# Optimization experiments

Hardware: AMD Instinct MI355X
Metric: run time of the kernel (lower is better)

The kernel has to match this reference:

```python
import jax, jax.numpy as jnp
import numpy as np
from jax import lax

EPS = 1e-05
Q = 4          # window size (hard-coded in BotBlock)
HEADS = 4
DIM = 16       # bottleneck(64) // heads(4)


def conv3x3(x, w, b):
    # x: [N,C,H,W], w: [O,I,3,3]
    y = lax.conv_general_dilated(x, w, (1, 1), ((1, 1), (1, 1)),
                                 dimension_numbers=('NCHW', 'OIHW', 'NCHW'))
    return y + b[None, :, None, None]


def batchnorm(x, gamma, beta):
    # training-mode BN: batch statistics over (N,H,W), biased variance
    m = jnp.mean(x, axis=(0, 2, 3), keepdims=True)
    v = jnp.var(x, axis=(0, 2, 3), keepdims=True)
    xn = (x - m) * lax.rsqrt(v + EPS)
    return xn * gamma[None, :, None, None] + beta[None, :, None, None]


def rel_to_abs(x):
    # x: [B, H, L, 2L-1] -> [B, H, L, L] via pad/reshape trick
    B, H, L, _ = x.shape
    x = jnp.pad(x, ((0, 0), (0, 0), (0, 0), (0, 1)))          # [B,H,L,2L]
    flat = x.reshape(B, H, -1)                                  # [B,H,2L*L]
    flat = jnp.pad(flat, ((0, 0), (0, 0), (0, L - 1)))
    final = flat.reshape(B, H, L + 1, 2 * L - 1)
    return final[:, :, :L, L - 1:]                              # [B,H,L,L]


def relative_logits_1d(q, rel_k, perm):
    # q: [b, n, h, w, d], rel_k: [2w-1, d]
    b, n, h, w, d = q.shape
    rl = jnp.einsum('bnhwd,md->bnhwm', q, rel_k)
    rl = rl.reshape(b, n * h, w, 2 * w - 1)
    rl = rel_to_abs(rl)                                         # [b, n*h, w, w]
    rl = rl.reshape(b, n, h, w, w)
    rl = jnp.broadcast_to(rl[:, :, :, None], (b, n, h, h, w, w))
    return jnp.transpose(rl, perm)


def rel_pos_attention(q, k, v, rel_w, rel_h):
    # q,k,v: [b, heads, h, w, d]
    b, n, h, w, d = q.shape
    q = q * (d ** -0.5)
    logits = jnp.einsum('bnhwd,bnpqd->bnhwpq', q, k)
    logits = logits + relative_logits_1d(q, rel_w, (0, 1, 2, 4, 3, 5))
    logits = logits + relative_logits_1d(jnp.transpose(q, (0, 1, 3, 2, 4)),
                                         rel_h, (0, 1, 4, 2, 5, 3))
    weights = jax.nn.softmax(logits.reshape(b, n, h, w, h * w), axis=-1)
    weights = weights.reshape(b, n, h, w, h, w)
    out = jnp.einsum('bnhwpq,bnpqd->bhwnd', weights, v)         # [b,h,w,n,d]
    return out.reshape(b, h, w, n * d)                          # fold heads


def setup_inputs() -> dict:
    key = jax.random.key(0)
    ks = jax.random.split(key, 16)
    C_in, C_bot, C_out = 64, 64, 256
    inp = {
        'x': jax.random.normal(ks[0], (2, C_in, 256, 256), jnp.float32),
        'conv1_w': jax.random.normal(ks[1], (C_bot, C_in, 3, 3), jnp.float32) * 0.05,
        'conv1_b': jnp.zeros((C_bot,), jnp.float32),
        'bn1_g': jnp.ones((C_bot,), jnp.float32),
        'bn1_b': jnp.zeros((C_bot,), jnp.float32),
        'wq': jax.random.normal(ks[2], (C_bot, HEADS, DIM), jnp.float32) * 0.01,
        'wk': jax.random.normal(ks[3], (C_bot, HEADS, DIM), jnp.float32) * 0.01,
        'wv': jax.random.normal(ks[4], (C_bot, HEADS, DIM), jnp.float32) * 0.01,
        'rel_w': jax.random.normal(ks[5], (2 * Q - 1, DIM), jnp.float32) * (DIM ** -0.5),
        'rel_h': jax.random.normal(ks[6], (2 * Q - 1, DIM), jnp.float32) * (DIM ** -0.5),
        'bn2_g': jnp.ones((C_bot,), jnp.float32),
        'bn2_b': jnp.zeros((C_bot,), jnp.float32),
        'conv3_w': jax.random.normal(ks[7], (C_out, C_bot, 3, 3), jnp.float32) * 0.05,
        'conv3_b': jnp.zeros((C_out,), jnp.float32),
        # NOTE: original init_zero=True zeros bn3 gamma; we randomize it so the
        # output (and gradients) are non-trivial for kernel correctness checks.
        'bn3_g': jax.random.normal(ks[8], (C_out,), jnp.float32),
        'bn3_b': jnp.zeros((C_out,), jnp.float32),
    }
    return inp


def reference(x, conv1_w, conv1_b, bn1_g, bn1_b, wq, wk, wv, rel_w, rel_h,
              bn2_g, bn2_b, conv3_w, conv3_b, bn3_g, bn3_b):
    N, C, H, W = x.shape
    P_h, P_w = H // Q, W // Q
    # raw memory reinterpretation into 4x4 blocks (matches torch .reshape)
    xb = x.reshape(N * P_h * P_w, C, Q, Q)
    out = jax.nn.relu(batchnorm(conv3x3(xb, conv1_w, conv1_b), bn1_g, bn1_b))
    # GroupPointWise projections: NCHW -> NHWC then einsum
    feat = jnp.transpose(out, (0, 2, 3, 1))                     # [b,h,w,c]
    q = jnp.einsum('bhwc,cnp->bnhwp', feat, wq)
    k = jnp.einsum('bhwc,cnp->bnhwp', feat, wk)
    v = jnp.einsum('bhwc,cnp->bnhwp', feat, wv)
    o = rel_pos_attention(q, k, v, rel_w, rel_h)                # [b,h,w,c]
    o = jnp.transpose(o, (0, 3, 1, 2))                          # NCHW
    o = jax.nn.relu(batchnorm(o, bn2_g, bn2_b))
    o = batchnorm(conv3x3(o, conv3_w, conv3_b), bn3_g, bn3_b)   # no act
    C1 = o.shape[1]
    o = o.reshape(N, C1, H, W)
    return jax.nn.relu(o)
```

## Files before the change

kernel.cpp:

```cpp
#include <hip/hip_runtime.h>
#include <stdint.h>


#define EPSV 1e-5f
#define INV_N (1.0f / 131072.0f)

typedef unsigned short u16;
typedef __attribute__((ext_vector_type(8))) short short8b;
typedef __attribute__((ext_vector_type(4))) short short4b;
typedef __attribute__((ext_vector_type(4))) float f32x4;

__device__ __forceinline__ u16 f2bf(float f) {
  unsigned u = __float_as_uint(f);
  u += 0x7fffu + ((u >> 16) & 1u);
  return (u16)(u >> 16);
}
__device__ __forceinline__ float bf2f(u16 h) {
  return __uint_as_float((unsigned)h << 16);
}
__device__ __forceinline__ unsigned cvtpk(float lo, float hi) {
  unsigned r;
  asm("v_cvt_pk_bf16_f32 %0, %1, %2" : "=v"(r) : "v"(lo), "v"(hi));
  return r;
}
__device__ __forceinline__ short4b pack4(unsigned lo, unsigned hi) {
  union { unsigned u[2]; short4b s; } x;
  x.u[0] = lo; x.u[1] = hi;
  return x.s;
}
__device__ __forceinline__ f32x4 mfma16(short4b a, short4b b, f32x4 c) {
#if __has_builtin(__builtin_amdgcn_mfma_f32_16x16x16_bf16)
  return __builtin_amdgcn_mfma_f32_16x16x16_bf16(a, b, c, 0, 0, 0);
#elif __has_builtin(__builtin_amdgcn_mfma_f32_16x16x16bf16_1k)
  return __builtin_amdgcn_mfma_f32_16x16x16bf16_1k(a, b, c, 0, 0, 0);
#else
  f32x4 d;
  asm volatile("v_mfma_f32_16x16x16_bf16 %0, %1, %2, %3\n\ts_nop 7\n\ts_nop 7"
               : "=v"(d) : "v"(a), "v"(b), "v"(c));
  return d;
#endif
}

__device__ __forceinline__ float bn_scale(const float* __restrict__ acc,
                                          const float* __restrict__ gam,
                                          const float* __restrict__ bet,
                                          int C, int c, float& shift) {
  float S = acc[c], S2 = acc[C + c];
  float mean = S * INV_N;
  float var  = S2 * INV_N - mean * mean;
  float rstd = rsqrtf(var + EPSV);
  float sc = gam[c] * rstd;
  shift = bet[c] - mean * sc;
  return sc;
}

__global__ __launch_bounds__(256) void prep_kernel(const float* __restrict__ w1,
                                                   const float* __restrict__ w3,
                                                   const float* __restrict__ wq,
                                                   const float* __restrict__ wk,
                                                   const float* __restrict__ wv,
                                                   const float* __restrict__ relw,
                                                   const float* __restrict__ relh,
                                                   u16* __restrict__ wp1,
                                                   u16* __restrict__ wp3,
                                                   u16* __restrict__ wqkvT) {
  int i = blockIdx.x * 256 + threadIdx.x;
  const int tot1 = 18 * 64 * 40;
  const int tot3 = 9 * 256 * 64;
  if (i < tot1) {
    int ch = i / (64 * 40); int r = i - ch * 64 * 40; int o = r / 40; int kk = r - o * 40;
    float v = 0.f;
    if (kk < 32) { int k = ch * 32 + kk; int tap = k >> 6; int c = k & 63;
                   v = w1[o * 576 + c * 9 + tap]; }
    wp1[i] = f2bf(v);
  } else if (i < tot1 + tot3) {
    int j = i - tot1;
    int tap = j >> 14; int r = j & 16383; int o = r >> 6; int c = r & 63;
    wp3[j] = f2bf(w3[o * 576 + c * 9 + tap]);
  } else if (i < tot1 + tot3 + 192 * 64) {
    int j = i - tot1 - tot3;
    int oc = j >> 6, c = j & 63;
    const float* src = (oc < 64) ? wq : (oc < 128) ? wk : wv;
    float v = src[(c << 6) + (oc & 63)];
    if (oc < 64) v *= 0.25f;
    wqkvT[j] = f2bf(v);
  } else if (i < tot1 + tot3 + 192 * 64 + 4096) {
    int j = i - tot1 - tot3 - 192 * 64;
    int c = j & 63; int col = (j >> 6) & 31; int tbl = j >> 11;
    int n = col >> 3, m = col & 7;
    float v = 0.f;
    if (m < 7) {
      const float* rel = tbl ? relh : relw;
#pragma unroll
      for (int d = 0; d < 16; ++d) v += wq[c * 64 + n * 16 + d] * rel[m * 16 + d];
      v *= 0.25f;
    }
    wqkvT[(192 + tbl * 32 + col) * 64 + c] = f2bf(v);
  }
}

__global__ __launch_bounds__(256) void conv1_kernel(const float* __restrict__ x,
                                                    const u16* __restrict__ wp,
                                                    u16* __restrict__ bufb,
                                                    float* __restrict__ partials1) {
  __shared__ __align__(16) char featA[257 * 128];
  __shared__ __align__(16) char ldsW[2][64 * 80];
  const int t = threadIdx.x;
  const int lane = t & 63, w = t >> 6;
  const int lrow = lane & 15, lk = lane >> 4;
  const int wm = w >> 1, wn = w & 1;
  const size_t Mbase = (size_t)blockIdx.x * 256;

  int rel[9];
  {
    const int pi = lrow >> 2, pj = lrow & 3;
#pragma unroll
    for (int tap = 0; tap < 9; ++tap) {
      const int ti = tap / 3, tj = tap - ti * 3;
      int si = pi + ti - 1, sj = pj + tj - 1;
      bool valid = ((unsigned)si < 4u) && ((unsigned)sj < 4u);
      rel[tap] = valid ? ((si * 4 + sj) << 7) : (1 << 24);
    }
  }

  {
    const int cp = t >> 3, ph = t & 7;
    const int gsw = ((cp >> 2) << 4) | ((cp & 3) << 2);
#pragma unroll
    for (int i = 0; i < 16; ++i) {
      const float* bp = x + Mbase * 64 + i * 1024 + cp * 32 + ph * 2;
      float2 a = *reinterpret_cast<const float2*>(bp);
      float2 b = *reinterpret_cast<const float2*>(bp + 16);
#pragma unroll
      for (int j = 0; j < 2; ++j) {
        const int row = i * 16 + ph * 2 + j;
        unsigned pk = cvtpk(j ? a.y : a.x, j ? b.y : b.x);
        const int byte = row * 128 + (gsw ^ ((row & 7) << 4));
        *reinterpret_cast<unsigned*>(featA + byte) = pk;
      }
    }
  }
  if (t < 8) *reinterpret_cast<uint4*>(featA + 256 * 128 + t * 16) = uint4{0, 0, 0, 0};

  uint4 s0, s1;
  {
    const u16* sp = wp;
    s0 = *reinterpret_cast<const uint4*>(sp + (size_t)t * 8);
    if (t < 64) s1 = *reinterpret_cast<const uint4*>(sp + (size_t)(t + 256) * 8);
    *reinterpret_cast<uint4*>(ldsW[0] + t * 16) = s0;
    if (t < 64) *reinterpret_cast<uint4*>(ldsW[0] + (t + 256) * 16) = s1;
  }
  __syncthreads();

  f32x4 acc[8][2] = {};
#pragma unroll
  for (int chn = 0; chn < 18; ++chn) {
    const int cur = chn & 1;
    const int tap = chn >> 1, kk = chn & 1;
    if (chn + 1 < 18) {
      const u16* sp = wp + (chn + 1) * 2560;
      s0 = *reinterpret_cast<const uint4*>(sp + (size_t)t * 8);
      if (t < 64) s1 = *reinterpret_cast<const uint4*>(sp + (size_t)(t + 256) * 8);
    }
    const int kkg = (kk << 6) | (lk << 4);
    short8b bw[2];
#pragma unroll
    for (int n = 0; n < 2; ++n)
      bw[n] = *reinterpret_cast<const short8b*>(ldsW[cur] + (wn * 32 + n * 16 + lrow) * 80 + lk * 16);
#pragma unroll
    for (int m = 0; m < 8; ++m) {
      int ad = ((wm * 128 + m * 16) << 7) + rel[tap];
      ad = ad < 32768 ? ad : 32768;
      ad += (kkg ^ ((ad >> 3) & 0x70));
      short8b af = *reinterpret_cast<const short8b*>(featA + ad);
#pragma unroll
      for (int n = 0; n < 2; ++n)
        acc[m][n] = __builtin_amdgcn_mfma_f32_16x16x32_bf16(af, bw[n], acc[m][n], 0, 0, 0);
    }
    if (chn + 1 < 18) {
      *reinterpret_cast<uint4*>(ldsW[cur ^ 1] + t * 16) = s0;
      if (t < 64) *reinterpret_cast<uint4*>(ldsW[cur ^ 1] + (t + 256) * 16) = s1;
    }
    __syncthreads();
  }

#pragma unroll
  for (int m = 0; m < 8; ++m) {
    const size_t rowg0 = Mbase + wm * 128 + m * 16 + lk * 4;
#pragma unroll
    for (int n = 0; n < 2; ++n) {
      const int o = wn * 32 + n * 16 + lrow;
#pragma unroll
      for (int r = 0; r < 4; ++r)
        bufb[(rowg0 + r) * 64 + o] = f2bf(acc[m][n][r]);
    }
  }

  float* pst = reinterpret_cast<float*>(featA);
  if (t < 128) pst[t] = 0.f;
  __syncthreads();
#pragma unroll
  for (int n = 0; n < 2; ++n) {
    float s = 0.f, s2 = 0.f;
#pragma unroll
    for (int m = 0; m < 8; ++m)
#pragma unroll
      for (int r = 0; r < 4; ++r) {
        float v = acc[m][n][r];
        s += v; s2 = fmaf(v, v, s2);
      }
    s += __shfl_xor(s, 16); s2 += __shfl_xor(s2, 16);
    s += __shfl_xor(s, 32); s2 += __shfl_xor(s2, 32);
    if (lk == 0) {
      const int o = wn * 32 + n * 16 + lrow;
      atomicAdd(&pst[o], s);
      atomicAdd(&pst[64 + o], s2);
    }
  }
  __syncthreads();
  if (t < 128) partials1[(size_t)blockIdx.x * 128 + t] = pst[t];
}

__global__ __launch_bounds__(256) void reduce12_kernel(const float* __restrict__ p,
                                                       float* __restrict__ acc, int nrows) {
  const int c = blockIdx.x, t = threadIdx.x;
  float s = 0.f;
  for (int i = t; i < nrows; i += 256) s += p[(size_t)i * 128 + c];
#pragma unroll
  for (int off = 32; off > 0; off >>= 1) s += __shfl_down(s, off);
  __shared__ float red[4];
  if ((t & 63) == 0) red[t >> 6] = s;
  __syncthreads();
  if (t == 0) acc[c] = red[0] + red[1] + red[2] + red[3];
}

__global__ __launch_bounds__(256) void attn_kernel(u16* __restrict__ buf,
                                                   const u16* __restrict__ wqkvT,
                                                   const float* __restrict__ acc1,
                                                   const float* __restrict__ g1,
                                                   const float* __restrict__ b1,
                                                   float* __restrict__ partials2) {
  __shared__ float scsh[64][2];
  __shared__ float pstA[128];
  __shared__ __align__(16) u16 feat_l[4][1024];
  __shared__ __align__(16) float S_lds[4][16 * 18];
  __shared__ __align__(16) u16 V_lds[4][16 * 20];
  __shared__ __align__(16) float inv_lds[4][16];
  __shared__ __align__(16) u16 rLs[4][1152];
  const int t = threadIdx.x, u = t >> 6, lane = t & 63;
  const size_t b = (size_t)blockIdx.x * 4 + u;
  const int lrow = lane & 15, lk = lane >> 4;
  float* Sl = S_lds[u];
  u16* Vl = V_lds[u];
  float* invl = inv_lds[u];
  u16* rL = rLs[u];

  if (t < 64) {
    float sh; float sc = bn_scale(acc1, g1, b1, 64, t, sh);
    scsh[t][0] = sc; scsh[t][1] = sh;
  }
  if (t < 128) pstA[t] = 0.f;
  __syncthreads();

  {
    const int pos = lane >> 2, cq = lane & 3;
    const u16* src = buf + b * 1024 + pos * 64 + cq * 16;
    short8b v0 = *reinterpret_cast<const short8b*>(src);
    short8b v1 = *reinterpret_cast<const short8b*>(src + 8);
    float f[16];
#pragma unroll
    for (int j = 0; j < 8; ++j) {
      const int c0 = cq * 16 + j, c1 = cq * 16 + 8 + j;
      f[j]     = fmaxf(fmaf(bf2f((u16)v0[j]), scsh[c0][0], scsh[c0][1]), 0.f);
      f[8 + j] = fmaxf(fmaf(bf2f((u16)v1[j]), scsh[c1][0], scsh[c1][1]), 0.f);
    }
    uint4 q0{cvtpk(f[0], f[1]), cvtpk(f[2], f[3]), cvtpk(f[4], f[5]), cvtpk(f[6], f[7])};
    uint4 q1{cvtpk(f[8], f[9]), cvtpk(f[10], f[11]), cvtpk(f[12], f[13]), cvtpk(f[14], f[15])};
    const int g0 = (cq * 2) ^ (pos & 7), g1g = (cq * 2 + 1) ^ (pos & 7);
    *reinterpret_cast<uint4*>(&feat_l[u][pos * 64 + g0 * 8]) = q0;
    *reinterpret_cast<uint4*>(&feat_l[u][pos * 64 + g1g * 8]) = q1;
  }

  short8b bfeat[2];
#pragma unroll
  for (int ch = 0; ch < 2; ++ch) {
    const int kg = ch * 4 + lk;
    bfeat[ch] = *reinterpret_cast<const short8b*>(&feat_l[u][lrow * 64 + ((kg ^ (lrow & 7)) * 8)]);
  }
  short4b qf[4], kf[4];
  uint2 vf[4];
#pragma unroll
  for (int ct = 0; ct < 16; ++ct) {
    f32x4 d = {0.f, 0.f, 0.f, 0.f};
#pragma unroll
    for (int ch = 0; ch < 2; ++ch) {
      short8b wfr = *reinterpret_cast<const short8b*>(&wqkvT[(ct * 16 + lrow) * 64 + ch * 32 + lk * 8]);
      d = __builtin_amdgcn_mfma_f32_16x16x32_bf16(wfr, bfeat[ch], d, 0, 0, 0);
    }
    if (ct < 4) {
      qf[ct] = pack4(cvtpk(d[0], d[1]), cvtpk(d[2], d[3]));
    } else if (ct < 8) {
      kf[ct - 4] = pack4(cvtpk(d[0], d[1]), cvtpk(d[2], d[3]));
    } else if (ct < 12) {
      vf[ct - 8] = uint2{cvtpk(d[0], d[1]), cvtpk(d[2], d[3])};
    } else {
#pragma unroll
      for (int r = 0; r < 4; ++r) {
        const int rc = (ct - 12) * 16 + lk * 4 + r;
        const int tbl = rc >> 5, col = rc & 31;
        rL[tbl * 576 + (col >> 3) * 144 + lrow * 9 + (col & 7)] = f2bf(d[r]);
      }
    }
  }

  const f32x4 fzero = {0.f, 0.f, 0.f, 0.f};
  const int qj3 = 3 - (lrow & 3);
  const int qi = lrow >> 2;
#pragma unroll
  for (int n = 0; n < 4; ++n) {
    f32x4 S = mfma16(qf[n], kf[n], fzero);
#pragma unroll
    for (int r = 0; r < 4; ++r) Sl[(lk * 4 + r) * 18 + lrow] = S[r];
    const float* srow = Sl + lrow * 18 + lk * 4;
    float2 sa = *reinterpret_cast<const float2*>(srow);
    float2 sb = *reinterpret_cast<const float2*>(srow + 2);
    float s0 = sa.x, s1 = sa.y, s2 = sb.x, s3 = sb.y;
    const u16* rwp = rL + n * 144 + lrow * 9 + qj3;
    const float rh = bf2f(rL[576 + n * 144 + lrow * 9 + 3 + lk - qi]);
    s0 += bf2f(rwp[0]) + rh; s1 += bf2f(rwp[1]) + rh;
    s2 += bf2f(rwp[2]) + rh; s3 += bf2f(rwp[3]) + rh;
    float m = fmaxf(fmaxf(s0, s1), fmaxf(s2, s3));
    m = fmaxf(m, __shfl_xor(m, 16)); m = fmaxf(m, __shfl_xor(m, 32));
    float p0 = __expf(s0 - m), p1 = __expf(s1 - m);
    float p2 = __expf(s2 - m), p3 = __expf(s3 - m);
    float ls = p0 + p1 + p2 + p3;
    ls += __shfl_xor(ls, 16); ls += __shfl_xor(ls, 32);
    if (lk == 0) invl[lrow] = 1.f / ls;
    short4b pf = pack4(cvtpk(p0, p1), cvtpk(p2, p3));
    *reinterpret_cast<uint2*>(Vl + lrow * 20 + lk * 4) = vf[n];
    const int vb = lk * 4;
    unsigned v0 = Vl[(vb + 0) * 20 + lrow], v1 = Vl[(vb + 1) * 20 + lrow];
    unsigned v2 = Vl[(vb + 2) * 20 + lrow], v3 = Vl[(vb + 3) * 20 + lrow];
    short4b vB = pack4(v0 | (v1 << 16), v2 | (v3 << 16));
    f32x4 O = mfma16(pf, vB, fzero);
    float4 iv = *reinterpret_cast<const float4*>(invl + lk * 4);
    float o0 = O[0] * iv.x, o1 = O[1] * iv.y, o2 = O[2] * iv.z, o3 = O[3] * iv.w;
    u16* ob = buf + b * 1024 + (n << 4) + lrow;
    ob[(lk * 4 + 0) * 64] = f2bf(o0); ob[(lk * 4 + 1) * 64] = f2bf(o1);
    ob[(lk * 4 + 2) * 64] = f2bf(o2); ob[(lk * 4 + 3) * 64] = f2bf(o3);
    float ss = o0 + o1 + o2 + o3;
    float s2s = o0 * o0 + o1 * o1 + o2 * o2 + o3 * o3;
    ss += __shfl_xor(ss, 16); s2s += __shfl_xor(s2s, 16);
    ss += __shfl_xor(ss, 32); s2s += __shfl_xor(s2s, 32);
    if (lk == 0) {
      atomicAdd(&pstA[(n << 4) + lrow], ss);
      atomicAdd(&pstA[64 + (n << 4) + lrow], s2s);
    }
  }
  __syncthreads();
  if (t < 128) partials2[(size_t)blockIdx.x * 128 + t] = pstA[t];
}

__global__ __launch_bounds__(256, 2) void conv3_kernel(const u16* __restrict__ src,
                                                       const u16* __restrict__ wp,
                                                       const float* __restrict__ acc2,
                                                       const float* __restrict__ g2,
                                                       const float* __restrict__ b2,
                                                       u16* __restrict__ y3b,
                                                       float* __restrict__ partials3) {
  __shared__ __align__(16) u16 featB[257 * 64];
  __shared__ __align__(16) u16 ldsW[2][128 * 64];
  __shared__ float scsh[128];
  __shared__ __align__(16) u16 Tl[4][16 * 20];
  const int t = threadIdx.x;
  const int lane = t & 63, w = t >> 6;
  const int lrow = lane & 15, lk = lane >> 4;
  const int wm = w >> 1, wn = w & 1;
  const int Nbase = blockIdx.x * 256;
  const int ohalf = blockIdx.y;

  int rel[9];
  {
    const int pi = lrow >> 2, pj = lrow & 3;
#pragma unroll
    for (int tap = 0; tap < 9; ++tap) {
      const int ti = tap / 3, tj = tap - ti * 3;
      int si = pi + ti - 1, sj = pj + tj - 1;
      bool valid = ((unsigned)si < 4u) && ((unsigned)sj < 4u);
      rel[tap] = valid ? ((si * 4 + sj) << 7) : (1 << 24);
    }
  }
  if (t < 64) {
    float sh; float sc = bn_scale(acc2, g2, b2, 64, t, sh);
    scsh[t * 2] = sc; scsh[t * 2 + 1] = sh;
  }
  const int so = t >> 1, shalf = t & 1, so7 = so & 7;
  {
    const u16* wsrc = wp + ohalf * 8192 + so * 64 + shalf * 32;
    uint4 w0 = *reinterpret_cast<const uint4*>(wsrc);
    uint4 w1 = *reinterpret_cast<const uint4*>(wsrc + 8);
    uint4 w2 = *reinterpret_cast<const uint4*>(wsrc + 16);
    uint4 w3v = *reinterpret_cast<const uint4*>(wsrc + 24);
    char* dst = (char*)ldsW[0] + so * 128;
    const int gb = shalf * 4;
    *reinterpret_cast<uint4*>(dst + (((gb + 0) ^ so7) << 4)) = w0;
    *reinterpret_cast<uint4*>(dst + (((gb + 1) ^ so7) << 4)) = w1;
    *reinterpret_cast<uint4*>(dst + (((gb + 2) ^ so7) << 4)) = w2;
    *reinterpret_cast<uint4*>(dst + (((gb + 3) ^ so7) << 4)) = w3v;
  }
  __syncthreads();
  {
    const u16* srow = src + (size_t)(Nbase + t) * 64;
    char* drow = (char*)featB + t * 128;
    const int r7 = t & 7;
#pragma unroll
    for (int g = 0; g < 8; ++g) {
      short8b v = *reinterpret_cast<const short8b*>(srow + g * 8);
      float f[8];
#pragma unroll
      for (int j = 0; j < 8; ++j) {
        const int c = g * 8 + j;
        f[j] = fmaxf(fmaf(bf2f((u16)v[j]), scsh[c * 2], scsh[c * 2 + 1]), 0.f);
      }
      uint4 pk{cvtpk(f[0], f[1]), cvtpk(f[2], f[3]), cvtpk(f[4], f[5]), cvtpk(f[6], f[7])};
      *reinterpret_cast<uint4*>(drow + ((g ^ r7) << 4)) = pk;
    }
  }
  if (t < 8) *reinterpret_cast<uint4*>((char*)featB + 32768 + t * 16) = uint4{0, 0, 0, 0};
  uint4 r0, r1, r2, r3v;
  {
    const u16* wsrc = wp + 16384 + ohalf * 8192 + so * 64 + shalf * 32;
    r0 = *reinterpret_cast<const uint4*>(wsrc);
    r1 = *reinterpret_cast<const uint4*>(wsrc + 8);
    r2 = *reinterpret_cast<const uint4*>(wsrc + 16);
    r3v = *reinterpret_cast<const uint4*>(wsrc + 24);
  }
  __syncthreads();
  f32x4 acc[4][8] = {};
  const char* fB = (const char*)featB;
  const int swzA0 = (lk << 4) ^ ((lrow & 7) << 4);
  const int swzA1 = (64 | (lk << 4)) ^ ((lrow & 7) << 4);
#pragma unroll
  for (int tap = 0; tap < 9; ++tap) {
    const int cur = tap & 1;
    const char* lW = (const char*)ldsW[cur];
    short8b aw0[4], aw1[4];
#pragma unroll
    for (int m = 0; m < 4; ++m) {
      const int rowoff = (wm * 64 + m * 16 + lrow) << 7;
      aw0[m] = *reinterpret_cast<const short8b*>(lW + rowoff + swzA0);
      aw1[m] = *reinterpret_cast<const short8b*>(lW + rowoff + swzA1);
    }
#pragma unroll
    for (int n = 0; n < 8; ++n) {
      int ad0 = ((wn * 128 + n * 16) << 7) + rel[tap];
      ad0 = ad0 < 32768 ? ad0 : 32768;
      const int swz = (ad0 >> 3) & 0x70;
      short8b bf0 = *reinterpret_cast<const short8b*>(fB + ad0 + ((lk << 4) ^ swz));
      short8b bf1 = *reinterpret_cast<const short8b*>(fB + ad0 + ((64 | (lk << 4)) ^ swz));
#pragma unroll
      for (int m = 0; m < 4; ++m) {
        acc[m][n] = __builtin_amdgcn_mfma_f32_16x16x32_bf16(aw0[m], bf0, acc[m][n], 0, 0, 0);
        acc[m][n] = __builtin_amdgcn_mfma_f32_16x16x32_bf16(aw1[m], bf1, acc[m][n], 0, 0, 0);
      }
    }
    if (tap < 8) {
      char* dst = (char*)ldsW[cur ^ 1] + so * 128;
      const int gb = shalf * 4;
      *reinterpret_cast<uint4*>(dst + (((gb + 0) ^ so7) << 4)) = r0;
      *reinterpret_cast<uint4*>(dst + (((gb + 1) ^ so7) << 4)) = r1;
      *reinterpret_cast<uint4*>(dst + (((gb + 2) ^ so7) << 4)) = r2;
      *reinterpret_cast<uint4*>(dst + (((gb + 3) ^ so7) << 4)) = r3v;
      if (tap < 7) {
        const u16* wsrc = wp + (tap + 2) * 16384 + ohalf * 8192 + so * 64 + shalf * 32;
        r0 = *reinterpret_cast<const uint4*>(wsrc);
        r1 = *reinterpret_cast<const uint4*>(wsrc + 8);
        r2 = *reinterpret_cast<const uint4*>(wsrc + 16);
        r3v = *reinterpret_cast<const uint4*>(wsrc + 24);
      }
    }
    __syncthreads();
  }

  {
    u16* tl = Tl[w];
#pragma unroll
    for (int m = 0; m < 4; ++m) {
      const int o0 = ohalf * 128 + wm * 64 + m * 16;
#pragma unroll
      for (int n = 0; n < 8; ++n) {
#pragma unroll
        for (int r = 0; r < 4; ++r)
          tl[(lk * 4 + r) * 20 + lrow] = f2bf(acc[m][n][r]);
        const int bidx = (Nbase + wn * 128 + n * 16) >> 4;
        uint2 pk = *reinterpret_cast<const uint2*>(&tl[lrow * 20 + lk * 4]);
        *reinterpret_cast<uint2*>(y3b + (size_t)bidx * 4096 +
                                  (size_t)(o0 + lrow) * 16 + lk * 4) = pk;
      }
    }
  }

  float* pst = reinterpret_cast<float*>(featB);
  pst[t] = 0.f;
  __syncthreads();
#pragma unroll
  for (int m = 0; m < 4; ++m) {
#pragma unroll
    for (int r = 0; r < 4; ++r) {
      float s = 0.f, s2 = 0.f;
#pragma unroll
      for (int n = 0; n < 8; ++n) {
        float v = acc[m][n][r];
        s += v; s2 = fmaf(v, v, s2);
      }
      s += __shfl_xor(s, 1); s2 += __shfl_xor(s2, 1);
      s += __shfl_xor(s, 2); s2 += __shfl_xor(s2, 2);
      s += __shfl_xor(s, 4); s2 += __shfl_xor(s2, 4);
      s += __shfl_xor(s, 8); s2 += __shfl_xor(s2, 8);
      if (lrow == 0) {
        const int ch = wm * 64 + m * 16 + lk * 4 + r;
        atomicAdd(&pst[ch], s);
        atomicAdd(&pst[128 + ch], s2);
      }
    }
  }
  __syncthreads();
  partials3[((size_t)(ohalf * 512 + blockIdx.x)) * 256 + t] = pst[t];
}

__global__ __launch_bounds__(256) void reduce3_kernel(const float* __restrict__ p,
                                                      float* __restrict__ acc3) {
  const int c2 = blockIdx.x, t = threadIdx.x;
  const int kind = c2 >> 8, c = c2 & 255;
  const int h = c >> 7, chl = c & 127;
  float s = 0.f;
  for (int i = t; i < 512; i += 256)
    s += p[((size_t)(h * 512 + i)) * 256 + kind * 128 + chl];
#pragma unroll
  for (int off = 32; off > 0; off >>= 1) s += __shfl_down(s, off);
  __shared__ float red[4];
  if ((t & 63) == 0) red[t >> 6] = s;
  __syncthreads();
  if (t == 0) acc3[kind * 256 + c] = red[0] + red[1] + red[2] + red[3];
}

__global__ __launch_bounds__(256) void final_kernel(const u16* __restrict__ y3b,
                                                    float* __restrict__ out,
                                                    const float* __restrict__ acc3,
                                                    const float* __restrict__ g3,
                                                    const float* __restrict__ b3) {
  const size_t i = ((size_t)blockIdx.x * 256 + threadIdx.x) * 8;
  const int c = (int)((i >> 4) & 255);
  float sh; const float sc = bn_scale(acc3, g3, b3, 256, c, sh);
  short8b v = *reinterpret_cast<const short8b*>(y3b + i);
  float4 o0, o1;
  o0.x = fmaxf(fmaf(bf2f((u16)v[0]), sc, sh), 0.f);
  o0.y = fmaxf(fmaf(bf2f((u16)v[1]), sc, sh), 0.f);
  o0.z = fmaxf(fmaf(bf2f((u16)v[2]), sc, sh), 0.f);
  o0.w = fmaxf(fmaf(bf2f((u16)v[3]), sc, sh), 0.f);
  o1.x = fmaxf(fmaf(bf2f((u16)v[4]), sc, sh), 0.f);
  o1.y = fmaxf(fmaf(bf2f((u16)v[5]), sc, sh), 0.f);
  o1.z = fmaxf(fmaf(bf2f((u16)v[6]), sc, sh), 0.f);
  o1.w = fmaxf(fmaf(bf2f((u16)v[7]), sc, sh), 0.f);
  *reinterpret_cast<float4*>(out + i) = o0;
  *reinterpret_cast<float4*>(out + i + 4) = o1;
}

extern "C" void kernel_launch(void* const* d_in, const int* in_sizes, int n_in,
                              void* d_out, int out_size, void* d_ws, size_t ws_size,
                              hipStream_t stream) {
  const float* x   = (const float*)d_in[0];
  const float* w1  = (const float*)d_in[1];
  const float* g1  = (const float*)d_in[3];
  const float* bb1 = (const float*)d_in[4];
  const float* wq  = (const float*)d_in[5];
  const float* wk  = (const float*)d_in[6];
  const float* wv  = (const float*)d_in[7];
  const float* rw  = (const float*)d_in[8];
  const float* rh  = (const float*)d_in[9];
  const float* g2  = (const float*)d_in[10];
  const float* bb2 = (const float*)d_in[11];
  const float* w3  = (const float*)d_in[12];
  const float* g3  = (const float*)d_in[14];
  const float* bb3 = (const float*)d_in[15];
  float* out = (float*)d_out;
  float* ws  = (float*)d_ws;

  u16*   bufb   = (u16*)ws;
  u16*   y3     = bufb + 8388608;
  u16*   wp1    = y3 + 33554432;
  u16*   wp3    = wp1 + 46080;
  u16*   wqkvT  = wp3 + 147456;
  float* acc1   = ws + 21076480;
  float* acc2   = acc1 + 128;
  float* acc3   = acc2 + 128;
  float* part1  = acc3 + 512;
  float* part2  = part1 + 65536;
  float* part3  = part2 + 262144;

  prep_kernel<<<820, 256, 0, stream>>>(w1, w3, wq, wk, wv, rw, rh, wp1, wp3, wqkvT);
  conv1_kernel<<<512, 256, 0, stream>>>(x, wp1, bufb, part1);
  reduce12_kernel<<<128, 256, 0, stream>>>(part1, acc1, 512);
  attn_kernel<<<2048, 256, 0, stream>>>(bufb, wqkvT, acc1, g1, bb1, part2);
  reduce12_kernel<<<128, 256, 0, stream>>>(part2, acc2, 2048);
  conv3_kernel<<<dim3(512, 2), 256, 0, stream>>>(bufb, wp3, acc2, g2, bb2, y3, part3);
  reduce3_kernel<<<512, 256, 0, stream>>>(part3, acc3);
  final_kernel<<<16384, 256, 0, stream>>>(y3, out, acc3, g3, bb3);
}
```

Before: 157.5 us.

## Load conv weight fragments straight from global memory instead of LDS staging

In both conv1 and conv3, the double-buffered shared-memory staging of weights and the per-tap block barriers are removed. Each wave now reads its MFMA weight fragments directly from global memory, relying on the cache since every block reads the same small weight set. The conv1 weight layout drops the 40-element padding to 32, and conv1 gets a launch bound hint for occupancy. This cuts LDS use and synchronisation, at the cost of global loads with more latency inside the MFMA loop.

```diff
diff --git a/kernel.cpp b/kernel.cpp
--- a/kernel.cpp
+++ b/kernel.cpp
@@ -65,14 +65,12 @@
                                                    u16* __restrict__ wp3,
                                                    u16* __restrict__ wqkvT) {
   int i = blockIdx.x * 256 + threadIdx.x;
-  const int tot1 = 18 * 64 * 40;
+  const int tot1 = 18 * 64 * 32;
   const int tot3 = 9 * 256 * 64;
   if (i < tot1) {
-    int ch = i / (64 * 40); int r = i - ch * 64 * 40; int o = r / 40; int kk = r - o * 40;
-    float v = 0.f;
-    if (kk < 32) { int k = ch * 32 + kk; int tap = k >> 6; int c = k & 63;
-                   v = w1[o * 576 + c * 9 + tap]; }
-    wp1[i] = f2bf(v);
+    int ch = i >> 11; int r = i & 2047; int o = r >> 5; int kk = r & 31;
+    int k = ch * 32 + kk; int tap = k >> 6; int c = k & 63;
+    wp1[i] = f2bf(w1[o * 576 + c * 9 + tap]);
   } else if (i < tot1 + tot3) {
     int j = i - tot1;
     int tap = j >> 14; int r = j & 16383; int o = r >> 6; int c = r & 63;
@@ -99,12 +97,11 @@
   }
 }
 
-__global__ __launch_bounds__(256) void conv1_kernel(const float* __restrict__ x,
-                                                    const u16* __restrict__ wp,
-                                                    u16* __restrict__ bufb,
-                                                    float* __restrict__ partials1) {
+__global__ __launch_bounds__(256, 3) void conv1_kernel(const float* __restrict__ x,
+                                                       const u16* __restrict__ wp,
+                                                       u16* __restrict__ bufb,
+                                                       float* __restrict__ partials1) {
   __shared__ __align__(16) char featA[257 * 128];
-  __shared__ __align__(16) char ldsW[2][64 * 80];
   const int t = threadIdx.x;
   const int lane = t & 63, w = t >> 6;
   const int lrow = lane & 15, lk = lane >> 4;
@@ -141,32 +138,18 @@
     }
   }
   if (t < 8) *reinterpret_cast<uint4*>(featA + 256 * 128 + t * 16) = uint4{0, 0, 0, 0};
-
-  uint4 s0, s1;
-  {
-    const u16* sp = wp;
-    s0 = *reinterpret_cast<const uint4*>(sp + (size_t)t * 8);
-    if (t < 64) s1 = *reinterpret_cast<const uint4*>(sp + (size_t)(t + 256) * 8);
-    *reinterpret_cast<uint4*>(ldsW[0] + t * 16) = s0;
-    if (t < 64) *reinterpret_cast<uint4*>(ldsW[0] + (t + 256) * 16) = s1;
-  }
   __syncthreads();
 
   f32x4 acc[8][2] = {};
 #pragma unroll
   for (int chn = 0; chn < 18; ++chn) {
-    const int cur = chn & 1;
     const int tap = chn >> 1, kk = chn & 1;
-    if (chn + 1 < 18) {
-      const u16* sp = wp + (chn + 1) * 2560;
-      s0 = *reinterpret_cast<const uint4*>(sp + (size_t)t * 8);
-      if (t < 64) s1 = *reinterpret_cast<const uint4*>(sp + (size_t)(t + 256) * 8);
-    }
     const int kkg = (kk << 6) | (lk << 4);
     short8b bw[2];
 #pragma unroll
     for (int n = 0; n < 2; ++n)
-      bw[n] = *reinterpret_cast<const short8b*>(ldsW[cur] + (wn * 32 + n * 16 + lrow) * 80 + lk * 16);
+      bw[n] = *reinterpret_cast<const short8b*>(wp + chn * 2048 +
+                                                (wn * 32 + n * 16 + lrow) * 32 + lk * 8);
 #pragma unroll
     for (int m = 0; m < 8; ++m) {
       int ad = ((wm * 128 + m * 16) << 7) + rel[tap];
@@ -177,11 +160,6 @@
       for (int n = 0; n < 2; ++n)
         acc[m][n] = __builtin_amdgcn_mfma_f32_16x16x32_bf16(af, bw[n], acc[m][n], 0, 0, 0);
     }
-    if (chn + 1 < 18) {
-      *reinterpret_cast<uint4*>(ldsW[cur ^ 1] + t * 16) = s0;
-      if (t < 64) *reinterpret_cast<uint4*>(ldsW[cur ^ 1] + (t + 256) * 16) = s1;
-    }
-    __syncthreads();
   }
 
 #pragma unroll
@@ -196,6 +174,7 @@
     }
   }
 
+  __syncthreads();
   float* pst = reinterpret_cast<float*>(featA);
   if (t < 128) pst[t] = 0.f;
   __syncthreads();
@@ -369,7 +348,6 @@
                                                        u16* __restrict__ y3b,
                                                        float* __restrict__ partials3) {
   __shared__ __align__(16) u16 featB[257 * 64];
-  __shared__ __align__(16) u16 ldsW[2][128 * 64];
   __shared__ float scsh[128];
   __shared__ __align__(16) u16 Tl[4][16 * 20];
   const int t = threadIdx.x;
@@ -394,21 +372,8 @@
     float sh; float sc = bn_scale(acc2, g2, b2, 64, t, sh);
     scsh[t * 2] = sc; scsh[t * 2 + 1] = sh;
   }
-  const int so = t >> 1, shalf = t & 1, so7 = so & 7;
-  {
-    const u16* wsrc = wp + ohalf * 8192 + so * 64 + shalf * 32;
-    uint4 w0 = *reinterpret_cast<const uint4*>(wsrc);
-    uint4 w1 = *reinterpret_cast<const uint4*>(wsrc + 8);
-    uint4 w2 = *reinterpret_cast<const uint4*>(wsrc + 16);
-    uint4 w3v = *reinterpret_cast<const uint4*>(wsrc + 24);
-    char* dst = (char*)ldsW[0] + so * 128;
-    const int gb = shalf * 4;
-    *reinterpret_cast<uint4*>(dst + (((gb + 0) ^ so7) << 4)) = w0;
-    *reinterpret_cast<uint4*>(dst + (((gb + 1) ^ so7) << 4)) = w1;
-    *reinterpret_cast<uint4*>(dst + (((gb + 2) ^ so7) << 4)) = w2;
-    *reinterpret_cast<uint4*>(dst + (((gb + 3) ^ so7) << 4)) = w3v;
-  }
-  __syncthreads();
+  __syncthreads();
+
   {
     const u16* srow = src + (size_t)(Nbase + t) * 64;
     char* drow = (char*)featB + t * 128;
@@ -427,29 +392,20 @@
     }
   }
   if (t < 8) *reinterpret_cast<uint4*>((char*)featB + 32768 + t * 16) = uint4{0, 0, 0, 0};
-  uint4 r0, r1, r2, r3v;
-  {
-    const u16* wsrc = wp + 16384 + ohalf * 8192 + so * 64 + shalf * 32;
-    r0 = *reinterpret_cast<const uint4*>(wsrc);
-    r1 = *reinterpret_cast<const uint4*>(wsrc + 8);
-    r2 = *reinterpret_cast<const uint4*>(wsrc + 16);
-    r3v = *reinterpret_cast<const uint4*>(wsrc + 24);
-  }
-  __syncthreads();
+  __syncthreads();
+
   f32x4 acc[4][8] = {};
   const char* fB = (const char*)featB;
-  const int swzA0 = (lk << 4) ^ ((lrow & 7) << 4);
-  const int swzA1 = (64 | (lk << 4)) ^ ((lrow & 7) << 4);
+  const u16* wbase = wp + (size_t)(ohalf * 128 + wm * 64) * 64;
+
 #pragma unroll
   for (int tap = 0; tap < 9; ++tap) {
-    const int cur = tap & 1;
-    const char* lW = (const char*)ldsW[cur];
     short8b aw0[4], aw1[4];
 #pragma unroll
     for (int m = 0; m < 4; ++m) {
-      const int rowoff = (wm * 64 + m * 16 + lrow) << 7;
-      aw0[m] = *reinterpret_cast<const short8b*>(lW + rowoff + swzA0);
-      aw1[m] = *reinterpret_cast<const short8b*>(lW + rowoff + swzA1);
+      const u16* wrow = wbase + (size_t)tap * 16384 + (m * 16 + lrow) * 64;
+      aw0[m] = *reinterpret_cast<const short8b*>(wrow + lk * 8);
+      aw1[m] = *reinterpret_cast<const short8b*>(wrow + 32 + lk * 8);
     }
 #pragma unroll
     for (int n = 0; n < 8; ++n) {
@@ -464,22 +420,6 @@
         acc[m][n] = __builtin_amdgcn_mfma_f32_16x16x32_bf16(aw1[m], bf1, acc[m][n], 0, 0, 0);
       }
     }
-    if (tap < 8) {
-      char* dst = (char*)ldsW[cur ^ 1] + so * 128;
-      const int gb = shalf * 4;
-      *reinterpret_cast<uint4*>(dst + (((gb + 0) ^ so7) << 4)) = r0;
-      *reinterpret_cast<uint4*>(dst + (((gb + 1) ^ so7) << 4)) = r1;
-      *reinterpret_cast<uint4*>(dst + (((gb + 2) ^ so7) << 4)) = r2;
-      *reinterpret_cast<uint4*>(dst + (((gb + 3) ^ so7) << 4)) = r3v;
-      if (tap < 7) {
-        const u16* wsrc = wp + (tap + 2) * 16384 + ohalf * 8192 + so * 64 + shalf * 32;
-        r0 = *reinterpret_cast<const uint4*>(wsrc);
-        r1 = *reinterpret_cast<const uint4*>(wsrc + 8);
-        r2 = *reinterpret_cast<const uint4*>(wsrc + 16);
-        r3v = *reinterpret_cast<const uint4*>(wsrc + 24);
-      }
-    }
-    __syncthreads();
   }
 
   {
@@ -500,6 +440,7 @@
     }
   }
 
+  __syncthreads();
   float* pst = reinterpret_cast<float*>(featB);
   pst[t] = 0.f;
   __syncthreads();
@@ -589,16 +530,16 @@
   u16*   bufb   = (u16*)ws;
   u16*   y3     = bufb + 8388608;
   u16*   wp1    = y3 + 33554432;
-  u16*   wp3    = wp1 + 46080;
+  u16*   wp3    = wp1 + 36864;
   u16*   wqkvT  = wp3 + 147456;
-  float* acc1   = ws + 21076480;
+  float* acc1   = ws + 21071872;
   float* acc2   = acc1 + 128;
   float* acc3   = acc2 + 128;
   float* part1  = acc3 + 512;
   float* part2  = part1 + 65536;
   float* part3  = part2 + 262144;
 
-  prep_kernel<<<820, 256, 0, stream>>>(w1, w3, wq, wk, wv, rw, rh, wp1, wp3, wqkvT);
+  prep_kernel<<<784, 256, 0, stream>>>(w1, w3, wq, wk, wv, rw, rh, wp1, wp3, wqkvT);
   conv1_kernel<<<512, 256, 0, stream>>>(x, wp1, bufb, part1);
   reduce12_kernel<<<128, 256, 0, stream>>>(part1, acc1, 512);
   attn_kernel<<<2048, 256, 0, stream>>>(bufb, wqkvT, acc1, g1, bb1, part2);
```

After: 166.7 us. 1.06x slower.
